# Kernel tuning notes

Measured on AMD Instinct MI355X. Metric: run time of the kernel, lower is better.

The kernel has to match this reference:

```python
import jax, jax.numpy as jnp
from jax import lax
import numpy as np


def _farthest_point_sample(points, num_centroids):
    """points: [B, C, N] float. Returns int32 indices [B, num_centroids].

    Standard PointNet++ CUDA semantics: start from point index 0, maintain a
    running min squared distance to the selected set, pick argmax each step.
    """
    B, C, N = points.shape

    def step(carry, _):
        min_dist, farthest = carry  # [B, N], [B]
        # gather current centroid coords: [B, C, 1]
        centroid = jnp.take_along_axis(points, farthest[:, None, None], axis=2)
        d = jnp.sum((points - centroid) ** 2, axis=1)  # [B, N]
        min_dist = jnp.minimum(min_dist, d)
        nxt = jnp.argmax(min_dist, axis=1).astype(jnp.int32)  # [B]
        return (min_dist, nxt), farthest

    init = (jnp.full((B, N), jnp.finfo(points.dtype).max, points.dtype),
            jnp.zeros((B,), jnp.int32))
    _, idx = lax.scan(step, init, None, length=num_centroids)  # idx: [S, B]
    return idx.T  # [B, num_centroids]


def setup_inputs() -> dict:
    key = jax.random.key(0)
    B, C, N = 32, 3, 131072
    points = jax.random.normal(key, (B, C, N), dtype=jnp.float32)
    return {"points": points, "num_centroids": 2048}


def reference(points, num_centroids):
    return _farthest_point_sample(points, num_centroids)
```

## Files before the change

kernel.cpp:

```cpp
#include <hip/hip_runtime.h>
#include <stdint.h>

typedef unsigned long long u64;

#define NBATCH 32
#define NPTS   131072
#define KBLK   8
#define PPB    (NPTS / KBLK)
#define NTHR   1024
#define NWAVE  (NTHR / 64)
#define PPT    (PPB / NTHR)
#define FLT_MAX_C 3.402823466e+38f

__device__ __forceinline__ u64* slot_ptr(u64* slots, int b, int k, int par) {
    return slots + ((size_t)((b * KBLK + k) * 2 + par)) * 8;
}

__global__ __launch_bounds__(NTHR, 4)
void fps_kernel(const float* __restrict__ points, int* __restrict__ out,
                u64* __restrict__ slots, int S)
{
    const int b    = blockIdx.x & (NBATCH - 1);
    const int kk   = blockIdx.x >> 5;
    const int t    = threadIdx.x;
    const int lane = t & 63;
    const int wv   = t >> 6;

    const float* pb = points + (size_t)b * 3 * NPTS;
    const float* bx = pb + kk * PPB;
    const float* by = bx + NPTS;
    const float* bz = bx + 2 * NPTS;

    float px[PPT], py[PPT], pz[PPT], md[PPT];
    const int t4 = t * 4;
#pragma unroll
    for (int c = 0; c < PPT / 4; ++c) {
        float4 vx = *(const float4*)(bx + c * (NTHR * 4) + t4);
        float4 vy = *(const float4*)(by + c * (NTHR * 4) + t4);
        float4 vz = *(const float4*)(bz + c * (NTHR * 4) + t4);
        px[c*4+0]=vx.x; px[c*4+1]=vx.y; px[c*4+2]=vx.z; px[c*4+3]=vx.w;
        py[c*4+0]=vy.x; py[c*4+1]=vy.y; py[c*4+2]=vy.z; py[c*4+3]=vy.w;
        pz[c*4+0]=vz.x; pz[c*4+1]=vz.y; pz[c*4+2]=vz.z; pz[c*4+3]=vz.w;
        md[c*4+0]=FLT_MAX_C; md[c*4+1]=FLT_MAX_C;
        md[c*4+2]=FLT_MAX_C; md[c*4+3]=FLT_MAX_C;
    }

    __shared__ float s_v[NWAVE];
    __shared__ int   s_i[NWAVE];
    __shared__ int   s_bi;
    __shared__ unsigned s_bc[4];

    float cx = pb[0], cy = pb[NPTS], cz = pb[2 * NPTS];
    if (kk == 0 && t == 0) out[(size_t)b * S] = 0;

    for (int s = 1; s < S; ++s) {
        float bestv = -1.0f;
        int   bestp = 0;
#pragma unroll
        for (int p = 0; p < PPT; ++p) {
            float dx = __fsub_rn(px[p], cx);
            float dy = __fsub_rn(py[p], cy);
            float dz = __fsub_rn(pz[p], cz);
            float d  = __fadd_rn(__fadd_rn(__fmul_rn(dx, dx), __fmul_rn(dy, dy)),
                                 __fmul_rn(dz, dz));
            float m  = fminf(md[p], d);
            md[p] = m;
            bool tk = m > bestv;
            bestv = tk ? m : bestv;
            bestp = tk ? p : bestp;
        }
        int gidx = kk * PPB + (bestp >> 2) * (NTHR * 4) + t4 + (bestp & 3);

#pragma unroll
        for (int off = 32; off >= 1; off >>= 1) {
            float ov = __shfl_down(bestv, off);
            int   oi = __shfl_down(gidx, off);
            bool tk = (ov > bestv) || (ov == bestv && oi < gidx);
            bestv = tk ? ov : bestv;
            gidx  = tk ? oi : gidx;
        }
        if (lane == 0) { s_v[wv] = bestv; s_i[wv] = gidx; }
        __syncthreads();

        if (wv == 0) {
            float v16 = (lane < NWAVE) ? s_v[lane] : -1.0f;
            int   i16 = (lane < NWAVE) ? s_i[lane] : 0x7fffffff;
#pragma unroll
            for (int off = 8; off >= 1; off >>= 1) {
                float ov = __shfl_down(v16, off);
                int   oi = __shfl_down(i16, off);
                bool tk = (ov > v16) || (ov == v16 && oi < i16);
                v16 = tk ? ov : v16;
                i16 = tk ? oi : i16;
            }
            if (lane == 0) {
                u64 di = ((u64)(unsigned)s << 49)
                       | ((u64)__float_as_uint(v16) << 17)
                       | (u64)(unsigned)(131071 - i16);
                __hip_atomic_store(slot_ptr(slots, b, kk, s & 1) + 3, di,
                                   __ATOMIC_RELAXED, __HIP_MEMORY_SCOPE_AGENT);
                s_bi = i16;
            }
        }
        __syncthreads();

        int widx = s_bi;
        if ((widx >> 14) == kk) {
            int l = widx & (PPB - 1);
            if (t == ((l >> 2) & (NTHR - 1))) {
                int pw = ((l >> 12) << 2) | (l & 3);
                float wx = 0.f, wy = 0.f, wz = 0.f;
#pragma unroll
                for (int p = 0; p < PPT; ++p) {
                    bool e = (p == pw);
                    wx = e ? px[p] : wx; wy = e ? py[p] : wy; wz = e ? pz[p] : wz;
                }
                u64 tg = (u64)(unsigned)s << 32;
                u64* sp = slot_ptr(slots, b, kk, s & 1);
                __hip_atomic_store(sp + 0, tg | __float_as_uint(wx),
                                   __ATOMIC_RELAXED, __HIP_MEMORY_SCOPE_AGENT);
                __hip_atomic_store(sp + 1, tg | __float_as_uint(wy),
                                   __ATOMIC_RELAXED, __HIP_MEMORY_SCOPE_AGENT);
                __hip_atomic_store(sp + 2, tg | __float_as_uint(wz),
                                   __ATOMIC_RELAXED, __HIP_MEMORY_SCOPE_AGENT);
            }
        }

        if (wv == 0) {
            u64 got = 0;
            if (lane < 32) {
                u64* ps = slot_ptr(slots, b, lane >> 2, s & 1) + (lane & 3);
                const int sh = ((lane & 3) == 3) ? 49 : 32;
                do {
                    got = __hip_atomic_load(ps, __ATOMIC_RELAXED,
                                            __HIP_MEMORY_SCOPE_AGENT);
                } while ((int)(got >> sh) != s);
            }
            u64 dval = (u64)__shfl((long long)got, lane * 4 + 3);
            u64 dv = (lane < 8) ? dval : 0ull;
#pragma unroll
            for (int off = 4; off >= 1; off >>= 1) {
                u64 o = (u64)__shfl_down((long long)dv, off);
                dv = (o > dv) ? o : dv;
            }
            u64 win = (u64)__shfl((long long)dv, 0);
            u64 mask = __ballot(lane < 8 && dval == win);
            int w = __ffsll(mask) - 1;
            unsigned lo = (unsigned)got;
            unsigned cxb = (unsigned)__shfl((int)lo, w * 4 + 0);
            unsigned cyb = (unsigned)__shfl((int)lo, w * 4 + 1);
            unsigned czb = (unsigned)__shfl((int)lo, w * 4 + 2);
            int idx = 131071 - (int)(win & 0x1FFFF);
            if (lane == 0) {
                s_bc[0] = cxb; s_bc[1] = cyb; s_bc[2] = czb; s_bc[3] = (unsigned)idx;
                if (kk == 0) out[(size_t)b * S + s] = idx;
            }
        }
        __syncthreads();
        cx = __uint_as_float(s_bc[0]);
        cy = __uint_as_float(s_bc[1]);
        cz = __uint_as_float(s_bc[2]);
    }
}

extern "C" void kernel_launch(void* const* d_in, const int* in_sizes, int n_in,
                              void* d_out, int out_size, void* d_ws, size_t ws_size,
                              hipStream_t stream) {
    const float* points = (const float*)d_in[0];
    int* out   = (int*)d_out;
    u64* slots = (u64*)d_ws;
    int S = out_size / NBATCH;
    fps_kernel<<<dim3(NBATCH * KBLK), dim3(NTHR), 0, stream>>>(points, out, slots, S);
}
```

Before: 7.101 ms.

## Carry winner coordinates through reductions to drop a barrier and owner-publish step

The argmax reductions now also carry the winning point's xyz. Wave 0 can therefore publish coordinates and the packed distance/index in one place, which removes a __syncthreads and the owner-thread lookup that selected coordinates from the register arrays. Three quarters of the running min-distance array move from registers to shared memory to relieve register pressure. The cross-block reduction also switches to xor shuffles. The cost is extra shuffles for the coordinates and shared-memory traffic on every step.

```diff
diff --git a/kernel.cpp b/kernel.cpp
--- a/kernel.cpp
+++ b/kernel.cpp
@@ -6,10 +6,10 @@
 #define NBATCH 32
 #define NPTS   131072
 #define KBLK   8
-#define PPB    (NPTS / KBLK)
+#define PPB    16384
 #define NTHR   1024
-#define NWAVE  (NTHR / 64)
-#define PPT    (PPB / NTHR)
+#define NWAVE  16
+#define PPT    16
 #define FLT_MAX_C 3.402823466e+38f
 
 __device__ __forceinline__ u64* slot_ptr(u64* slots, int b, int k, int par) {
@@ -31,102 +31,124 @@
     const float* by = bx + NPTS;
     const float* bz = bx + 2 * NPTS;
 
-    float px[PPT], py[PPT], pz[PPT], md[PPT];
+    __shared__ float4 s_md[3][NTHR];
+    __shared__ float s_pv[NWAVE], s_px[NWAVE], s_py[NWAVE], s_pz[NWAVE];
+    __shared__ int   s_pi[NWAVE];
+    __shared__ unsigned s_bc[3];
+
+    float px[PPT], py[PPT], pz[PPT];
+    float4 mdr;
     const int t4 = t * 4;
+
 #pragma unroll
-    for (int c = 0; c < PPT / 4; ++c) {
+    for (int c = 0; c < 4; ++c) {
         float4 vx = *(const float4*)(bx + c * (NTHR * 4) + t4);
         float4 vy = *(const float4*)(by + c * (NTHR * 4) + t4);
         float4 vz = *(const float4*)(bz + c * (NTHR * 4) + t4);
         px[c*4+0]=vx.x; px[c*4+1]=vx.y; px[c*4+2]=vx.z; px[c*4+3]=vx.w;
         py[c*4+0]=vy.x; py[c*4+1]=vy.y; py[c*4+2]=vy.z; py[c*4+3]=vy.w;
         pz[c*4+0]=vz.x; pz[c*4+1]=vz.y; pz[c*4+2]=vz.z; pz[c*4+3]=vz.w;
-        md[c*4+0]=FLT_MAX_C; md[c*4+1]=FLT_MAX_C;
-        md[c*4+2]=FLT_MAX_C; md[c*4+3]=FLT_MAX_C;
     }
-
-    __shared__ float s_v[NWAVE];
-    __shared__ int   s_i[NWAVE];
-    __shared__ int   s_bi;
-    __shared__ unsigned s_bc[4];
+    {
+        float4 f4 = make_float4(FLT_MAX_C, FLT_MAX_C, FLT_MAX_C, FLT_MAX_C);
+        s_md[0][t] = f4; s_md[1][t] = f4; s_md[2][t] = f4; mdr = f4;
+    }
 
     float cx = pb[0], cy = pb[NPTS], cz = pb[2 * NPTS];
     if (kk == 0 && t == 0) out[(size_t)b * S] = 0;
 
     for (int s = 1; s < S; ++s) {
-        float bestv = -1.0f;
-        int   bestp = 0;
+        float bv = -1.0f; int bix = 0;
+        float bwx = 0.f, bwy = 0.f, bwz = 0.f;
+#define SCAN1(PXV, PYV, PZV, MREF, IDXC)                                    \
+        {                                                                   \
+            float dx = __fsub_rn(PXV, cx);                                  \
+            float dy = __fsub_rn(PYV, cy);                                  \
+            float dz = __fsub_rn(PZV, cz);                                  \
+            float d  = __fadd_rn(__fadd_rn(__fmul_rn(dx, dx),               \
+                                           __fmul_rn(dy, dy)),              \
+                                 __fmul_rn(dz, dz));                        \
+            float m  = fminf(MREF, d);                                      \
+            MREF = m;                                                       \
+            bool tk = m > bv;                                               \
+            bv  = tk ? m : bv;                                              \
+            bix = tk ? (IDXC) : bix;                                        \
+            bwx = tk ? (PXV) : bwx;                                         \
+            bwy = tk ? (PYV) : bwy;                                         \
+            bwz = tk ? (PZV) : bwz;                                         \
+        }
 #pragma unroll
-        for (int p = 0; p < PPT; ++p) {
-            float dx = __fsub_rn(px[p], cx);
-            float dy = __fsub_rn(py[p], cy);
-            float dz = __fsub_rn(pz[p], cz);
-            float d  = __fadd_rn(__fadd_rn(__fmul_rn(dx, dx), __fmul_rn(dy, dy)),
-                                 __fmul_rn(dz, dz));
-            float m  = fminf(md[p], d);
-            md[p] = m;
-            bool tk = m > bestv;
-            bestv = tk ? m : bestv;
-            bestp = tk ? p : bestp;
+        for (int c = 0; c < 3; ++c) {
+            float4 m4 = s_md[c][t];
+            SCAN1(px[c*4+0], py[c*4+0], pz[c*4+0], m4.x, c*4096 + t4 + 0);
+            SCAN1(px[c*4+1], py[c*4+1], pz[c*4+1], m4.y, c*4096 + t4 + 1);
+            SCAN1(px[c*4+2], py[c*4+2], pz[c*4+2], m4.z, c*4096 + t4 + 2);
+            SCAN1(px[c*4+3], py[c*4+3], pz[c*4+3], m4.w, c*4096 + t4 + 3);
+            s_md[c][t] = m4;
         }
-        int gidx = kk * PPB + (bestp >> 2) * (NTHR * 4) + t4 + (bestp & 3);
+        SCAN1(px[12], py[12], pz[12], mdr.x, 12288 + t4 + 0);
+        SCAN1(px[13], py[13], pz[13], mdr.y, 12288 + t4 + 1);
+        SCAN1(px[14], py[14], pz[14], mdr.z, 12288 + t4 + 2);
+        SCAN1(px[15], py[15], pz[15], mdr.w, 12288 + t4 + 3);
+#undef SCAN1
 
 #pragma unroll
         for (int off = 32; off >= 1; off >>= 1) {
-            float ov = __shfl_down(bestv, off);
-            int   oi = __shfl_down(gidx, off);
-            bool tk = (ov > bestv) || (ov == bestv && oi < gidx);
-            bestv = tk ? ov : bestv;
-            gidx  = tk ? oi : gidx;
+            float ov = __shfl_down(bv, off);
+            int   oi = __shfl_down(bix, off);
+            float ox = __shfl_down(bwx, off);
+            float oy = __shfl_down(bwy, off);
+            float oz = __shfl_down(bwz, off);
+            bool tk = (ov > bv) || (ov == bv && oi < bix);
+            bv  = tk ? ov : bv;
+            bix = tk ? oi : bix;
+            bwx = tk ? ox : bwx;
+            bwy = tk ? oy : bwy;
+            bwz = tk ? oz : bwz;
         }
-        if (lane == 0) { s_v[wv] = bestv; s_i[wv] = gidx; }
+        if (lane == 0) {
+            s_pv[wv] = bv; s_pi[wv] = bix;
+            s_px[wv] = bwx; s_py[wv] = bwy; s_pz[wv] = bwz;
+        }
         __syncthreads();
 
         if (wv == 0) {
-            float v16 = (lane < NWAVE) ? s_v[lane] : -1.0f;
-            int   i16 = (lane < NWAVE) ? s_i[lane] : 0x7fffffff;
+            float v16 = (lane < NWAVE) ? s_pv[lane] : -1.0f;
+            int   i16 = (lane < NWAVE) ? s_pi[lane] : 0x7fffffff;
+            float x16 = (lane < NWAVE) ? s_px[lane] : 0.f;
+            float y16 = (lane < NWAVE) ? s_py[lane] : 0.f;
+            float z16 = (lane < NWAVE) ? s_pz[lane] : 0.f;
 #pragma unroll
             for (int off = 8; off >= 1; off >>= 1) {
                 float ov = __shfl_down(v16, off);
                 int   oi = __shfl_down(i16, off);
+                float ox = __shfl_down(x16, off);
+                float oy = __shfl_down(y16, off);
+                float oz = __shfl_down(z16, off);
                 bool tk = (ov > v16) || (ov == v16 && oi < i16);
                 v16 = tk ? ov : v16;
                 i16 = tk ? oi : i16;
+                x16 = tk ? ox : x16;
+                y16 = tk ? oy : y16;
+                z16 = tk ? oz : z16;
             }
             if (lane == 0) {
+                int g = kk * PPB + i16;
+                u64* sp = slot_ptr(slots, b, kk, s & 1);
+                u64 tg = (u64)(unsigned)s << 32;
                 u64 di = ((u64)(unsigned)s << 49)
                        | ((u64)__float_as_uint(v16) << 17)
-                       | (u64)(unsigned)(131071 - i16);
-                __hip_atomic_store(slot_ptr(slots, b, kk, s & 1) + 3, di,
+                       | (u64)(unsigned)(131071 - g);
+                __hip_atomic_store(sp + 0, tg | __float_as_uint(x16),
                                    __ATOMIC_RELAXED, __HIP_MEMORY_SCOPE_AGENT);
-                s_bi = i16;
-            }
-        }
-        __syncthreads();
-
-        int widx = s_bi;
-        if ((widx >> 14) == kk) {
-            int l = widx & (PPB - 1);
-            if (t == ((l >> 2) & (NTHR - 1))) {
-                int pw = ((l >> 12) << 2) | (l & 3);
-                float wx = 0.f, wy = 0.f, wz = 0.f;
-#pragma unroll
-                for (int p = 0; p < PPT; ++p) {
-                    bool e = (p == pw);
-                    wx = e ? px[p] : wx; wy = e ? py[p] : wy; wz = e ? pz[p] : wz;
-                }
-                u64 tg = (u64)(unsigned)s << 32;
-                u64* sp = slot_ptr(slots, b, kk, s & 1);
-                __hip_atomic_store(sp + 0, tg | __float_as_uint(wx),
+                __hip_atomic_store(sp + 1, tg | __float_as_uint(y16),
                                    __ATOMIC_RELAXED, __HIP_MEMORY_SCOPE_AGENT);
-                __hip_atomic_store(sp + 1, tg | __float_as_uint(wy),
+                __hip_atomic_store(sp + 2, tg | __float_as_uint(z16),
                                    __ATOMIC_RELAXED, __HIP_MEMORY_SCOPE_AGENT);
-                __hip_atomic_store(sp + 2, tg | __float_as_uint(wz),
+                __hip_atomic_store(sp + 3, di,
                                    __ATOMIC_RELAXED, __HIP_MEMORY_SCOPE_AGENT);
             }
-        }
 
-        if (wv == 0) {
             u64 got = 0;
             if (lane < 32) {
                 u64* ps = slot_ptr(slots, b, lane >> 2, s & 1) + (lane & 3);
@@ -136,24 +158,22 @@
                                             __HIP_MEMORY_SCOPE_AGENT);
                 } while ((int)(got >> sh) != s);
             }
-            u64 dval = (u64)__shfl((long long)got, lane * 4 + 3);
-            u64 dv = (lane < 8) ? dval : 0ull;
+            u64 dval = (u64)__shfl((long long)got, ((lane & 7) << 2) | 3);
+            u64 dv = dval;
 #pragma unroll
-            for (int off = 4; off >= 1; off >>= 1) {
-                u64 o = (u64)__shfl_down((long long)dv, off);
+            for (int off = 1; off <= 4; off <<= 1) {
+                u64 o = (u64)__shfl_xor((long long)dv, off);
                 dv = (o > dv) ? o : dv;
             }
-            u64 win = (u64)__shfl((long long)dv, 0);
-            u64 mask = __ballot(lane < 8 && dval == win);
-            int w = __ffsll(mask) - 1;
+            u64 mask = __ballot(lane < 8 && dval == dv);
+            int w = __ffsll((long long)mask) - 1;
             unsigned lo = (unsigned)got;
             unsigned cxb = (unsigned)__shfl((int)lo, w * 4 + 0);
             unsigned cyb = (unsigned)__shfl((int)lo, w * 4 + 1);
             unsigned czb = (unsigned)__shfl((int)lo, w * 4 + 2);
-            int idx = 131071 - (int)(win & 0x1FFFF);
             if (lane == 0) {
-                s_bc[0] = cxb; s_bc[1] = cyb; s_bc[2] = czb; s_bc[3] = (unsigned)idx;
-                if (kk == 0) out[(size_t)b * S + s] = idx;
+                s_bc[0] = cxb; s_bc[1] = cyb; s_bc[2] = czb;
+                if (kk == 0) out[(size_t)b * S + s] = 131071 - (int)(dv & 0x1FFFF);
             }
         }
         __syncthreads();
```

New measurement: 8.946 ms. 1.26x slower.
